# Kernel optimization log

Measured on AMD Instinct MI355X. Metric: run time of the kernel, lower is better.

## Reference

```python
import jax, jax.numpy as jnp
import numpy as np

WIDTH_IN = 8
WIDTH_OUT = 8
STRIDES = (1, 1)
PADDING = 'SAME'


def quantizer(x, width, mode='round', clip=True):
    """Fixed-point quantization to `width` bits in [-1, 1), straight-through estimator.

    mode='round' -> round-to-nearest; mode='floor' -> truncate.
    clip=True saturates to the representable range [-1, 1 - 2^-(width-1)].
    """
    scale = jnp.asarray(2.0 ** (width - 1), x.dtype)
    q = jnp.round(x * scale) if mode == 'round' else jnp.floor(x * scale)
    q = q / scale
    # straight-through: forward uses q, gradient flows as identity
    q = x + jax.lax.stop_gradient(q - x)
    if clip:
        q = jnp.clip(q, -1.0, 1.0 - 1.0 / scale)
    return q


def setup_inputs() -> dict:
    key = jax.random.key(0)
    kx, kw = jax.random.split(key)
    x = jax.random.normal(kx, (32, 112, 112, 64), dtype=jnp.float32)      # NHWC
    kernels = jax.random.normal(kw, (3, 3, 64, 128), dtype=jnp.float32) * 0.05  # HWIO, RandomNormal init
    return {"x": x, "kernels": kernels}


def reference(x, kernels):
    # Method == 'Fixed' path of MyConv2D.call
    xq = quantizer(x, WIDTH_IN, 'round', clip=True)                # quantize activations
    kq = quantizer(kernels, WIDTH_IN, 'round', clip=True)          # quantize weights
    out = jax.lax.conv_general_dilated(
        xq, kq,
        window_strides=STRIDES,
        padding=PADDING,
        dimension_numbers=('NHWC', 'HWIO', 'NHWC'),
    )                                                              # [B, 112, 112, 128]
    out = quantizer(out, WIDTH_OUT, 'floor', clip=False)           # quantize output, truncating
    return out
```

## Files before the change

### kernel.cpp

```cpp
#include <hip/hip_runtime.h>

#define NIMG 32
#define H 112
#define W 112
#define CI 64
#define CO 128

typedef __attribute__((ext_vector_type(8))) __bf16 bf16x8;
typedef __attribute__((ext_vector_type(4))) float f32x4;
typedef __attribute__((ext_vector_type(4))) short short4v;
typedef __attribute__((ext_vector_type(4))) int int4v;

__device__ __forceinline__ short q8bits(float v) {
    float t = rintf(v * 128.0f);
    t = fminf(fmaxf(t, -128.0f), 127.0f);
    union { float f; unsigned u; } cv; cv.f = t;
    return (short)(cv.u >> 16);
}

__global__ __launch_bounds__(256) void quant_pack_w(const float* __restrict__ w,
                                                    short* __restrict__ bp) {
    int idx = blockIdx.x * 256 + threadIdx.x;
    int j    = idx & 7;
    int lane = (idx >> 3) & 63;
    int nt   = (idx >> 9) & 7;
    int kt   = idx >> 12;
    int k = kt * 32 + (lane >> 4) * 8 + j;
    int n = nt * 16 + (lane & 15);
    bp[idx] = q8bits(w[k * CO + n]);
}

__global__ __launch_bounds__(256) void quant_x(const float* __restrict__ x,
                                               short* __restrict__ xq) {
    size_t i = ((size_t)blockIdx.x * 256 + threadIdx.x) * 8;
    float4 v0 = *(const float4*)&x[i];
    float4 v1 = *(const float4*)&x[i + 4];
    short4v a, b;
    a.x = q8bits(v0.x); a.y = q8bits(v0.y); a.z = q8bits(v0.z); a.w = q8bits(v0.w);
    b.x = q8bits(v1.x); b.y = q8bits(v1.y); b.z = q8bits(v1.z); b.w = q8bits(v1.w);
    *(short4v*)&xq[i]     = a;
    *(short4v*)&xq[i + 4] = b;
}

#define LROW 7296

__global__ __launch_bounds__(256, 3) void conv1r(const short* __restrict__ xq,
                                                 const short* __restrict__ bp,
                                                 float* __restrict__ out) {
    __shared__ short xs[3 * LROW];
    int bid = blockIdx.x;
    int n = bid / H;
    int h = bid - n * H;
    int tid  = threadIdx.x;
    int lane = tid & 63;
    int wave = tid >> 6;

    int lc = lane >> 3;
    int jp = lane & 7;
    #pragma unroll
    for (int row = 0; row < 3; ++row) {
        short* ldsrow = &xs[row * LROW];
        int hr = h - 1 + row;
        if ((unsigned)hr < (unsigned)H) {
            const short* grow = xq + ((size_t)(n * H + hr) * W) * CI;
            for (int i = wave; i < 14; i += 4) {
                int gc = i * 8 + lc;
                int jl = jp ^ ((gc + 1) & 7);
                const short* g = grow + gc * 64 + jl * 8;
                __builtin_amdgcn_global_load_lds(
                    (const __attribute__((address_space(1))) void*)g,
                    (__attribute__((address_space(3))) void*)(ldsrow + 64 + i * 512),
                    16, 0, 0);
            }
        } else {
            for (int t = tid; t < 912; t += 256)
                *(int4v*)&ldsrow[t * 8] = (int4v){0, 0, 0, 0};
        }
    }
    if (wave == 3 && lane < 48) {
        int row = lane >> 4;
        int c = (lane & 8) ? 113 : 0;
        *(int4v*)&xs[row * LROW + c * 64 + (lane & 7) * 8] = (int4v){0, 0, 0, 0};
    }
    __syncthreads();

    int lane15 = lane & 15;
    int hi     = lane >> 4;
    int nt0    = wave * 2;

    const bf16x8* bfr = (const bf16x8*)bp;

    f32x4 acc[7][2];
    #pragma unroll
    for (int mt = 0; mt < 7; ++mt) {
        acc[mt][0] = (f32x4){0.f, 0.f, 0.f, 0.f};
        acc[mt][1] = (f32x4){0.f, 0.f, 0.f, 0.f};
    }

    #pragma unroll
    for (int r = 0; r < 3; ++r) {
        int rbase = r * LROW;
        #pragma unroll
        for (int s = 0; s < 3; ++s) {
            int cb = s + lane15;
            int sx = cb & 7;
            int abase = rbase + cb * 64;
            #pragma unroll
            for (int kh = 0; kh < 2; ++kh) {
                int kk = (r * 3 + s) * 2 + kh;
                bf16x8 b0 = bfr[(kk * 8 + nt0    ) * 64 + lane];
                bf16x8 b1 = bfr[(kk * 8 + nt0 + 1) * 64 + lane];
                int joff = ((kh * 4 + hi) ^ sx) * 8;
                #pragma unroll
                for (int mt = 0; mt < 7; ++mt) {
                    bf16x8 a = *(const bf16x8*)&xs[abase + mt * 1024 + joff];
                    acc[mt][0] = __builtin_amdgcn_mfma_f32_16x16x32_bf16(a, b0, acc[mt][0], 0, 0, 0);
                    acc[mt][1] = __builtin_amdgcn_mfma_f32_16x16x32_bf16(a, b1, acc[mt][1], 0, 0, 0);
                }
            }
        }
    }

    float* orow = out + (size_t)((n * H + h) * W) * CO;
    int co0  = wave * 32 + lane15;
    int rowb = hi * 4;
    #pragma unroll
    for (int mt = 0; mt < 7; ++mt)
        #pragma unroll
        for (int t = 0; t < 2; ++t)
            #pragma unroll
            for (int rg = 0; rg < 4; ++rg) {
                int m = mt * 16 + rowb + rg;
                orow[m * CO + co0 + t * 16] =
                    floorf(acc[mt][t][rg] * 0.0078125f) * 0.0078125f;
            }
}

#define LDSW 114
#define LDST 72
__global__ __launch_bounds__(256, 3) void conv_fb(const float* __restrict__ x,
                                                  const short* __restrict__ bp,
                                                  float* __restrict__ out) {
    __shared__ short xs[3 * LDSW * LDST];
    int bid = blockIdx.x;
    int n = bid / H;
    int h = bid - n * H;
    int tid = threadIdx.x;
    const float* xin = x + (size_t)n * (H * W * CI);
    for (int r = 0; r < 3; ++r) {
        int hrow = h + r - 1;
        bool rowok = ((unsigned)hrow < (unsigned)H);
        const float* srow = xin + (size_t)hrow * (W * CI);
        for (int t = tid; t < LDSW * 16; t += 256) {
            int c = t >> 4;
            int ci4 = (t & 15) << 2;
            int wcol = c - 1;
            float4 v = {0.f, 0.f, 0.f, 0.f};
            if (rowok && (unsigned)wcol < (unsigned)W)
                v = *(const float4*)&srow[wcol * CI + ci4];
            short4v sv;
            sv.x = q8bits(v.x); sv.y = q8bits(v.y);
            sv.z = q8bits(v.z); sv.w = q8bits(v.w);
            *(short4v*)&xs[(r * LDSW + c) * LDST + ci4] = sv;
        }
    }
    __syncthreads();
    int lane = tid & 63;
    int wave = tid >> 6;
    int laneoff = (lane & 15) * LDST + (lane >> 4) * 8;
    const bf16x8* bfr = (const bf16x8*)bp;
    int nt0 = wave * 2;
    f32x4 acc[7][2];
    #pragma unroll
    for (int mt = 0; mt < 7; ++mt) {
        acc[mt][0] = (f32x4){0.f, 0.f, 0.f, 0.f};
        acc[mt][1] = (f32x4){0.f, 0.f, 0.f, 0.f};
    }
    #pragma unroll
    for (int kk = 0; kk < 18; ++kk) {
        int rs = kk >> 1;
        int r = rs / 3;
        int s = rs - r * 3;
        bf16x8 b0 = bfr[(kk * 8 + nt0    ) * 64 + lane];
        bf16x8 b1 = bfr[(kk * 8 + nt0 + 1) * 64 + lane];
        int abase = (r * LDSW + s) * LDST + (kk & 1) * 32 + laneoff;
        #pragma unroll
        for (int mt = 0; mt < 7; ++mt) {
            bf16x8 a = *(const bf16x8*)&xs[abase + mt * 16 * LDST];
            acc[mt][0] = __builtin_amdgcn_mfma_f32_16x16x32_bf16(a, b0, acc[mt][0], 0, 0, 0);
            acc[mt][1] = __builtin_amdgcn_mfma_f32_16x16x32_bf16(a, b1, acc[mt][1], 0, 0, 0);
        }
    }
    float* orow = out + (size_t)(n * H + h) * (W * CO);
    int colc = wave * 32 + (lane & 15);
    int rowb = (lane >> 4) * 4;
    #pragma unroll
    for (int mt = 0; mt < 7; ++mt)
        #pragma unroll
        for (int t2 = 0; t2 < 2; ++t2)
            #pragma unroll
            for (int rg = 0; rg < 4; ++rg) {
                int m = mt * 16 + rowb + rg;
                orow[m * CO + colc + t2 * 16] =
                    floorf(acc[mt][t2][rg] * 0.0078125f) * 0.0078125f;
            }
}

extern "C" void kernel_launch(void* const* d_in, const int* in_sizes, int n_in,
                              void* d_out, int out_size, void* d_ws, size_t ws_size,
                              hipStream_t stream) {
    const float* x = (const float*)d_in[0];
    const float* w = (const float*)d_in[1];
    float* out = (float*)d_out;

    short* bp = (short*)d_ws;
    const size_t BP_BYTES = 147456;
    const size_t XQ_BYTES = (size_t)NIMG * H * W * CI * 2;
    quant_pack_w<<<288, 256, 0, stream>>>(w, bp);

    if (ws_size >= BP_BYTES + XQ_BYTES) {
        short* xqp = (short*)((char*)d_ws + BP_BYTES);
        quant_x<<<12544, 256, 0, stream>>>(x, xqp);
        conv1r<<<NIMG * H, 256, 0, stream>>>(xqp, bp, out);
    } else {
        conv_fb<<<NIMG * H, 256, 0, stream>>>(x, bp, out);
    }
}
```

Baseline: 340.3 us.

## Switch conv path to int8 MFMA with int8 quantized activations and weights

Quantized activations and weights are stored as exact int8 integers instead of bf16, and the convolution uses the i32_16x16x64_i8 MFMA. This halves the bytes of the intermediate activation tensor and LDS traffic, and doubles K per MFMA. All weights are held in registers for the whole block. Block IDs are remapped across XCDs, and the output is floored using an integer shift, which stays exact. In exchange, register pressure rises and the LDS swizzle is removed, which may bring back bank conflicts.

```diff
diff --git a/kernel.cpp b/kernel.cpp
--- a/kernel.cpp
+++ b/kernel.cpp
@@ -10,12 +10,131 @@
 typedef __attribute__((ext_vector_type(4))) float f32x4;
 typedef __attribute__((ext_vector_type(4))) short short4v;
 typedef __attribute__((ext_vector_type(4))) int int4v;
+typedef __attribute__((ext_vector_type(2))) int int2v;
 
 __device__ __forceinline__ short q8bits(float v) {
     float t = rintf(v * 128.0f);
     t = fminf(fmaxf(t, -128.0f), 127.0f);
     union { float f; unsigned u; } cv; cv.f = t;
     return (short)(cv.u >> 16);
+}
+__device__ __forceinline__ int q8i(float v) {
+    float t = rintf(v * 128.0f);
+    t = fminf(fmaxf(t, -128.0f), 127.0f);
+    return (int)t;
+}
+
+__global__ __launch_bounds__(256) void quant_pack_w_i8(const float* __restrict__ w,
+                                                       signed char* __restrict__ bp) {
+    int idx = blockIdx.x * 256 + threadIdx.x;
+    int j  = idx & 15;
+    int l  = (idx >> 4) & 63;
+    int nt = (idx >> 10) & 7;
+    int kk = idx >> 13;
+    int k = kk * 64 + (l >> 4) * 16 + j;
+    int n = nt * 16 + (l & 15);
+    bp[idx] = (signed char)q8i(w[k * CO + n]);
+}
+
+__global__ __launch_bounds__(256) void quant_x_i8(const float* __restrict__ x,
+                                                  signed char* __restrict__ xq) {
+    size_t i = ((size_t)blockIdx.x * 256 + threadIdx.x) * 8;
+    float4 v0 = *(const float4*)&x[i];
+    float4 v1 = *(const float4*)&x[i + 4];
+    int b0 = (q8i(v0.x) & 255) | ((q8i(v0.y) & 255) << 8) |
+             ((q8i(v0.z) & 255) << 16) | (q8i(v0.w) << 24);
+    int b1 = (q8i(v1.x) & 255) | ((q8i(v1.y) & 255) << 8) |
+             ((q8i(v1.z) & 255) << 16) | (q8i(v1.w) << 24);
+    int2v p; p.x = b0; p.y = b1;
+    *(int2v*)&xq[i] = p;
+}
+
+#define RB 7296
+
+__global__ __launch_bounds__(256, 3) void conv_i8(const signed char* __restrict__ xq,
+                                                  const signed char* __restrict__ bp,
+                                                  float* __restrict__ out) {
+    __shared__ __align__(16) signed char xs[3 * RB];
+    int bid0 = blockIdx.x;
+    int bid = (bid0 & 7) * 448 + (bid0 >> 3);
+    int n = bid / H;
+    int h = bid - n * H;
+    int tid  = threadIdx.x;
+    int lane = tid & 63;
+    int wave = tid >> 6;
+
+    const signed char* base = xq + (size_t)(n * H) * (W * CI);
+    for (int idx = wave; idx < 21; idx += 4) {
+        int row = idx / 7;
+        int i = idx - row * 7;
+        int hr = h - 1 + row;
+        if ((unsigned)hr < (unsigned)H) {
+            const signed char* g = base + (size_t)hr * (W * CI) + i * 1024 + lane * 16;
+            __builtin_amdgcn_global_load_lds(
+                (const __attribute__((address_space(1))) void*)g,
+                (__attribute__((address_space(3))) void*)(xs + row * RB + 64 + i * 1024),
+                16, 0, 0);
+        }
+    }
+
+    int nt0 = wave * 2;
+    const int4v* bp4 = (const int4v*)bp;
+    int4v breg[9][2];
+    #pragma unroll
+    for (int kk = 0; kk < 9; ++kk) {
+        breg[kk][0] = bp4[(kk * 8 + nt0    ) * 64 + lane];
+        breg[kk][1] = bp4[(kk * 8 + nt0 + 1) * 64 + lane];
+    }
+
+    if (h == 0)
+        for (int t = tid; t < 456; t += 256) *(int4v*)&xs[t * 16] = (int4v){0, 0, 0, 0};
+    if (h == H - 1)
+        for (int t = tid; t < 456; t += 256) *(int4v*)&xs[2 * RB + t * 16] = (int4v){0, 0, 0, 0};
+    if (tid < 24) {
+        int r2 = tid >> 3, ci = tid & 7;
+        int c = (ci & 4) ? 113 : 0;
+        *(int4v*)&xs[r2 * RB + c * 64 + (ci & 3) * 16] = (int4v){0, 0, 0, 0};
+    }
+    __syncthreads();
+
+    int lane15 = lane & 15;
+    int hi     = lane >> 4;
+
+    int4v acc[7][2];
+    #pragma unroll
+    for (int mt = 0; mt < 7; ++mt) {
+        acc[mt][0] = (int4v){0, 0, 0, 0};
+        acc[mt][1] = (int4v){0, 0, 0, 0};
+    }
+
+    #pragma unroll
+    for (int r = 0; r < 3; ++r) {
+        #pragma unroll
+        for (int s = 0; s < 3; ++s) {
+            int kk = r * 3 + s;
+            int abase = r * RB + (s + lane15) * 64 + hi * 16;
+            #pragma unroll
+            for (int mt = 0; mt < 7; ++mt) {
+                int4v a = *(const int4v*)&xs[abase + mt * 1024];
+                acc[mt][0] = __builtin_amdgcn_mfma_i32_16x16x64_i8(a, breg[kk][0], acc[mt][0], 0, 0, 0);
+                acc[mt][1] = __builtin_amdgcn_mfma_i32_16x16x64_i8(a, breg[kk][1], acc[mt][1], 0, 0, 0);
+            }
+        }
+    }
+
+    float* orow = out + (size_t)((n * H + h) * W) * CO;
+    int co0  = wave * 32 + lane15;
+    int rowb = hi * 4;
+    #pragma unroll
+    for (int mt = 0; mt < 7; ++mt)
+        #pragma unroll
+        for (int t = 0; t < 2; ++t)
+            #pragma unroll
+            for (int rg = 0; rg < 4; ++rg) {
+                int m = mt * 16 + rowb + rg;
+                orow[m * CO + co0 + t * 16] =
+                    (float)(acc[mt][t][rg] >> 7) * 0.0078125f;
+            }
 }
 
 __global__ __launch_bounds__(256) void quant_pack_w(const float* __restrict__ w,
@@ -28,112 +147,6 @@
     int k = kt * 32 + (lane >> 4) * 8 + j;
     int n = nt * 16 + (lane & 15);
     bp[idx] = q8bits(w[k * CO + n]);
-}
-
-__global__ __launch_bounds__(256) void quant_x(const float* __restrict__ x,
-                                               short* __restrict__ xq) {
-    size_t i = ((size_t)blockIdx.x * 256 + threadIdx.x) * 8;
-    float4 v0 = *(const float4*)&x[i];
-    float4 v1 = *(const float4*)&x[i + 4];
-    short4v a, b;
-    a.x = q8bits(v0.x); a.y = q8bits(v0.y); a.z = q8bits(v0.z); a.w = q8bits(v0.w);
-    b.x = q8bits(v1.x); b.y = q8bits(v1.y); b.z = q8bits(v1.z); b.w = q8bits(v1.w);
-    *(short4v*)&xq[i]     = a;
-    *(short4v*)&xq[i + 4] = b;
-}
-
-#define LROW 7296
-
-__global__ __launch_bounds__(256, 3) void conv1r(const short* __restrict__ xq,
-                                                 const short* __restrict__ bp,
-                                                 float* __restrict__ out) {
-    __shared__ short xs[3 * LROW];
-    int bid = blockIdx.x;
-    int n = bid / H;
-    int h = bid - n * H;
-    int tid  = threadIdx.x;
-    int lane = tid & 63;
-    int wave = tid >> 6;
-
-    int lc = lane >> 3;
-    int jp = lane & 7;
-    #pragma unroll
-    for (int row = 0; row < 3; ++row) {
-        short* ldsrow = &xs[row * LROW];
-        int hr = h - 1 + row;
-        if ((unsigned)hr < (unsigned)H) {
-            const short* grow = xq + ((size_t)(n * H + hr) * W) * CI;
-            for (int i = wave; i < 14; i += 4) {
-                int gc = i * 8 + lc;
-                int jl = jp ^ ((gc + 1) & 7);
-                const short* g = grow + gc * 64 + jl * 8;
-                __builtin_amdgcn_global_load_lds(
-                    (const __attribute__((address_space(1))) void*)g,
-                    (__attribute__((address_space(3))) void*)(ldsrow + 64 + i * 512),
-                    16, 0, 0);
-            }
-        } else {
-            for (int t = tid; t < 912; t += 256)
-                *(int4v*)&ldsrow[t * 8] = (int4v){0, 0, 0, 0};
-        }
-    }
-    if (wave == 3 && lane < 48) {
-        int row = lane >> 4;
-        int c = (lane & 8) ? 113 : 0;
-        *(int4v*)&xs[row * LROW + c * 64 + (lane & 7) * 8] = (int4v){0, 0, 0, 0};
-    }
-    __syncthreads();
-
-    int lane15 = lane & 15;
-    int hi     = lane >> 4;
-    int nt0    = wave * 2;
-
-    const bf16x8* bfr = (const bf16x8*)bp;
-
-    f32x4 acc[7][2];
-    #pragma unroll
-    for (int mt = 0; mt < 7; ++mt) {
-        acc[mt][0] = (f32x4){0.f, 0.f, 0.f, 0.f};
-        acc[mt][1] = (f32x4){0.f, 0.f, 0.f, 0.f};
-    }
-
-    #pragma unroll
-    for (int r = 0; r < 3; ++r) {
-        int rbase = r * LROW;
-        #pragma unroll
-        for (int s = 0; s < 3; ++s) {
-            int cb = s + lane15;
-            int sx = cb & 7;
-            int abase = rbase + cb * 64;
-            #pragma unroll
-            for (int kh = 0; kh < 2; ++kh) {
-                int kk = (r * 3 + s) * 2 + kh;
-                bf16x8 b0 = bfr[(kk * 8 + nt0    ) * 64 + lane];
-                bf16x8 b1 = bfr[(kk * 8 + nt0 + 1) * 64 + lane];
-                int joff = ((kh * 4 + hi) ^ sx) * 8;
-                #pragma unroll
-                for (int mt = 0; mt < 7; ++mt) {
-                    bf16x8 a = *(const bf16x8*)&xs[abase + mt * 1024 + joff];
-                    acc[mt][0] = __builtin_amdgcn_mfma_f32_16x16x32_bf16(a, b0, acc[mt][0], 0, 0, 0);
-                    acc[mt][1] = __builtin_amdgcn_mfma_f32_16x16x32_bf16(a, b1, acc[mt][1], 0, 0, 0);
-                }
-            }
-        }
-    }
-
-    float* orow = out + (size_t)((n * H + h) * W) * CO;
-    int co0  = wave * 32 + lane15;
-    int rowb = hi * 4;
-    #pragma unroll
-    for (int mt = 0; mt < 7; ++mt)
-        #pragma unroll
-        for (int t = 0; t < 2; ++t)
-            #pragma unroll
-            for (int rg = 0; rg < 4; ++rg) {
-                int m = mt * 16 + rowb + rg;
-                orow[m * CO + co0 + t * 16] =
-                    floorf(acc[mt][t][rg] * 0.0078125f) * 0.0078125f;
-            }
 }
 
 #define LDSW 114
@@ -213,16 +226,18 @@
     const float* w = (const float*)d_in[1];
     float* out = (float*)d_out;
 
-    short* bp = (short*)d_ws;
-    const size_t BP_BYTES = 147456;
-    const size_t XQ_BYTES = (size_t)NIMG * H * W * CI * 2;
-    quant_pack_w<<<288, 256, 0, stream>>>(w, bp);
-
-    if (ws_size >= BP_BYTES + XQ_BYTES) {
-        short* xqp = (short*)((char*)d_ws + BP_BYTES);
-        quant_x<<<12544, 256, 0, stream>>>(x, xqp);
-        conv1r<<<NIMG * H, 256, 0, stream>>>(xqp, bp, out);
+    const size_t BPI8_BYTES = 73728;
+    const size_t XQ8_BYTES  = (size_t)NIMG * H * W * CI;
+
+    if (ws_size >= BPI8_BYTES + XQ8_BYTES) {
+        signed char* bp8 = (signed char*)d_ws;
+        signed char* xq8 = (signed char*)d_ws + BPI8_BYTES;
+        quant_pack_w_i8<<<288, 256, 0, stream>>>(w, bp8);
+        quant_x_i8<<<12544, 256, 0, stream>>>(x, xq8);
+        conv_i8<<<NIMG * H, 256, 0, stream>>>(xq8, bp8, out);
     } else {
+        short* bp = (short*)d_ws;
+        quant_pack_w<<<288, 256, 0, stream>>>(w, bp);
         conv_fb<<<NIMG * H, 256, 0, stream>>>(x, bp, out);
     }
 }
```

Result: faster. 306.4 us (-9.9%).
